# Kernel optimization log

Measured on AMD Instinct MI355X. Metric: run time of the kernel, lower is better.

Reference implementation:

```python
import jax, jax.numpy as jnp
import numpy as np


def setup_inputs() -> dict:
    key = jax.random.key(0)
    k1, k2, k3, k4, k5, k6 = jax.random.split(key, 6)
    N, M = 4096, 4096      # data matrix
    K, D = 2048, 1024      # parameter matrix K x K, similarity matrix K x D
    Npair = 128            # size of i/j index subsets
    return {
        "actual": jax.random.normal(k1, (N, M), dtype=jnp.float32),
        "prediction": jax.random.normal(k2, (N, M), dtype=jnp.float32),
        "lamb": jnp.asarray(0.1, dtype=jnp.float32),
        "P": jax.random.normal(k3, (K, K), dtype=jnp.float32),
        "S": jax.random.normal(k4, (K, D), dtype=jnp.float32),
        "i_indices": jax.random.randint(k5, (Npair,), 0, K, dtype=jnp.int64),
        "j_indices": jax.random.randint(k6, (Npair,), 0, K, dtype=jnp.int64),
    }


def _safe_norm_rows(diff):
    # L2 norm over last axis with a zero-safe sqrt (grad is 0 at exactly-0 diffs,
    # matching torch's subgradient convention for .norm()).
    d2 = jnp.sum(diff * diff, axis=-1)
    pos = d2 > 0
    return jnp.sqrt(jnp.where(pos, d2, 1.0)) * pos


def reference(actual, prediction, lamb, P, S, i_indices, j_indices):
    # (p > 0) * clamp(p, min=0) == relu(p)
    Pp = jnp.maximum(P, 0.0)
    # penalty term: ||relu(P)||_F
    penalty = jnp.linalg.norm(Pp)
    # pairwise parameter-similarity penalty:
    # sum_{i in I, j in J} relu(P)[i,j] * || S[i,:] - S[j,:] ||_2
    Si = S[i_indices]                       # [Ni, D]
    Sj = S[j_indices]                       # [Nj, D]
    diff = Si[:, None, :] - Sj[None, :, :]  # [Ni, Nj, D]
    norms = _safe_norm_rows(diff)           # [Ni, Nj]
    Pij = Pp[i_indices[:, None], j_indices[None, :]]  # [Ni, Nj]
    parameter_penalty = jnp.sum(Pij * norms)
    data_term = jnp.linalg.norm(actual - prediction)
    return data_term + lamb * (penalty + parameter_penalty)
```

## Files before the change

kernel.cpp:

```cpp
#include <hip/hip_runtime.h>
#include <math.h>

#define BR 1024
#define BP 1024
#define TPB 256

__device__ __forceinline__ float waveReduceSum(float v) {
    #pragma unroll
    for (int off = 32; off > 0; off >>= 1)
        v += __shfl_down(v, off, 64);
    return v;
}

__global__ __launch_bounds__(256, 8)
void fused_kernel(const float* __restrict__ a,
                  const float* __restrict__ p,
                  const float* __restrict__ Pm,
                  const float* __restrict__ S,
                  const int* __restrict__ ii,
                  const int* __restrict__ jj,
                  float* __restrict__ ws,
                  long nAP, long nP, int Npair, int D, int K)
{
    __shared__ float sm0[4], sm1[4];
    const int wave = threadIdx.x >> 6;
    const int lane = threadIdx.x & 63;
    const int bid  = blockIdx.x;

    if (bid < BP) {
        const int totalPairs = Npair * Npair;
        const int base = bid * 16 + wave * 4;
        float local = 0.f;

        if (base < totalPairs && D == 1024 && (base % Npair) + 3 < Npair) {
            const int i  = base / Npair;
            const int j0 = base - i * Npair;
            const int ri = ii[i];
            const float4* Si4 = (const float4*)(S + (long)ri * D);
            float4 x0 = Si4[lane];
            float4 x1 = Si4[lane + 64];
            float4 x2 = Si4[lane + 128];
            float4 x3 = Si4[lane + 192];
            const long riK = (long)ri * K;

            float d2q[4];
            int   rjq[4];
            #pragma unroll
            for (int q = 0; q < 4; ++q) {
                const int rj = jj[j0 + q];
                rjq[q] = rj;
                const float4* Sj4 = (const float4*)(S + (long)rj * D);
                float4 y0 = Sj4[lane];
                float4 y1 = Sj4[lane + 64];
                float4 y2 = Sj4[lane + 128];
                float4 y3 = Sj4[lane + 192];
                float d2 = 0.f, e;
                e = x0.x - y0.x; d2 += e * e;
                e = x0.y - y0.y; d2 += e * e;
                e = x0.z - y0.z; d2 += e * e;
                e = x0.w - y0.w; d2 += e * e;
                e = x1.x - y1.x; d2 += e * e;
                e = x1.y - y1.y; d2 += e * e;
                e = x1.z - y1.z; d2 += e * e;
                e = x1.w - y1.w; d2 += e * e;
                e = x2.x - y2.x; d2 += e * e;
                e = x2.y - y2.y; d2 += e * e;
                e = x2.z - y2.z; d2 += e * e;
                e = x2.w - y2.w; d2 += e * e;
                e = x3.x - y3.x; d2 += e * e;
                e = x3.y - y3.y; d2 += e * e;
                e = x3.z - y3.z; d2 += e * e;
                e = x3.w - y3.w; d2 += e * e;
                d2q[q] = d2;
            }
            #pragma unroll
            for (int q = 0; q < 4; ++q)
                d2q[q] = waveReduceSum(d2q[q]);
            if (lane == 0) {
                #pragma unroll
                for (int q = 0; q < 4; ++q)
                    if (d2q[q] > 0.f)
                        local += fmaxf(Pm[riK + rjq[q]], 0.f) * sqrtf(d2q[q]);
            }
        } else {
            #pragma unroll
            for (int q = 0; q < 4; ++q) {
                int pair = base + q;
                if (pair < totalPairs) {
                    int i = pair / Npair;
                    int j = pair - i * Npair;
                    int ri = ii[i];
                    int rj = jj[j];
                    const float* Si = S + (long)ri * D;
                    const float* Sj = S + (long)rj * D;
                    float d2 = 0.f;
                    for (int c = lane; c < D; c += 64) {
                        float e = Si[c] - Sj[c];
                        d2 += e * e;
                    }
                    d2 = waveReduceSum(d2);
                    if (lane == 0 && d2 > 0.f)
                        local += fmaxf(Pm[(long)ri * K + rj], 0.f) * sqrtf(d2);
                }
            }
        }
        if (lane == 0) sm0[wave] = local;
        __syncthreads();
        if (threadIdx.x == 0)
            ws[2 * BR + bid] = sm0[0] + sm0[1] + sm0[2] + sm0[3];
    } else {
        const int rb = bid - BP;
        const long tid    = (long)rb * TPB + threadIdx.x;
        const long stride = (long)BR * TPB;

        const float4* a4 = (const float4*)a;
        const float4* p4 = (const float4*)p;
        long n4 = nAP >> 2;

        float s0a = 0.f, s0b = 0.f, s0c = 0.f, s0d = 0.f;
        long i = tid;
        for (; i + 3 * stride < n4; i += 4 * stride) {
            float4 av0 = a4[i];
            float4 av1 = a4[i + stride];
            float4 av2 = a4[i + 2 * stride];
            float4 av3 = a4[i + 3 * stride];
            float4 pv0 = p4[i];
            float4 pv1 = p4[i + stride];
            float4 pv2 = p4[i + 2 * stride];
            float4 pv3 = p4[i + 3 * stride];
            float d;
            d = av0.x - pv0.x; s0a += d * d;
            d = av0.y - pv0.y; s0a += d * d;
            d = av0.z - pv0.z; s0a += d * d;
            d = av0.w - pv0.w; s0a += d * d;
            d = av1.x - pv1.x; s0b += d * d;
            d = av1.y - pv1.y; s0b += d * d;
            d = av1.z - pv1.z; s0b += d * d;
            d = av1.w - pv1.w; s0b += d * d;
            d = av2.x - pv2.x; s0c += d * d;
            d = av2.y - pv2.y; s0c += d * d;
            d = av2.z - pv2.z; s0c += d * d;
            d = av2.w - pv2.w; s0c += d * d;
            d = av3.x - pv3.x; s0d += d * d;
            d = av3.y - pv3.y; s0d += d * d;
            d = av3.z - pv3.z; s0d += d * d;
            d = av3.w - pv3.w; s0d += d * d;
        }
        for (; i < n4; i += stride) {
            float4 av = a4[i], pv = p4[i];
            float d;
            d = av.x - pv.x; s0a += d * d;
            d = av.y - pv.y; s0a += d * d;
            d = av.z - pv.z; s0a += d * d;
            d = av.w - pv.w; s0a += d * d;
        }

        const float4* P4 = (const float4*)Pm;
        long nP4 = nP >> 2;
        float s1a = 0.f, s1b = 0.f;
        i = tid;
        for (; i + stride < nP4; i += 2 * stride) {
            float4 v0 = P4[i];
            float4 v1 = P4[i + stride];
            float r;
            r = fmaxf(v0.x, 0.f); s1a += r * r;
            r = fmaxf(v0.y, 0.f); s1a += r * r;
            r = fmaxf(v0.z, 0.f); s1a += r * r;
            r = fmaxf(v0.w, 0.f); s1a += r * r;
            r = fmaxf(v1.x, 0.f); s1b += r * r;
            r = fmaxf(v1.y, 0.f); s1b += r * r;
            r = fmaxf(v1.z, 0.f); s1b += r * r;
            r = fmaxf(v1.w, 0.f); s1b += r * r;
        }
        for (; i < nP4; i += stride) {
            float4 v = P4[i];
            float r;
            r = fmaxf(v.x, 0.f); s1a += r * r;
            r = fmaxf(v.y, 0.f); s1a += r * r;
            r = fmaxf(v.z, 0.f); s1a += r * r;
            r = fmaxf(v.w, 0.f); s1a += r * r;
        }

        float s0 = waveReduceSum(s0a + s0b + s0c + s0d);
        float s1 = waveReduceSum(s1a + s1b);
        if (lane == 0) { sm0[wave] = s0; sm1[wave] = s1; }
        __syncthreads();
        if (threadIdx.x == 0) {
            ws[rb]      = sm0[0] + sm0[1] + sm0[2] + sm0[3];
            ws[BR + rb] = sm1[0] + sm1[1] + sm1[2] + sm1[3];
        }
    }
}

__global__ void finalize_kernel(const float* __restrict__ ws,
                                const float* __restrict__ lamb,
                                float* __restrict__ out)
{
    float a0 = 0.f, a1 = 0.f, a2 = 0.f;
    for (int i = threadIdx.x; i < BR; i += TPB) {
        a0 += ws[i];
        a1 += ws[BR + i];
    }
    for (int i = threadIdx.x; i < BP; i += TPB)
        a2 += ws[2 * BR + i];

    a0 = waveReduceSum(a0);
    a1 = waveReduceSum(a1);
    a2 = waveReduceSum(a2);

    __shared__ float m0[4], m1[4], m2[4];
    int wave = threadIdx.x >> 6;
    int lane = threadIdx.x & 63;
    if (lane == 0) { m0[wave] = a0; m1[wave] = a1; m2[wave] = a2; }
    __syncthreads();
    if (threadIdx.x == 0) {
        float A0 = m0[0] + m0[1] + m0[2] + m0[3];
        float A1 = m1[0] + m1[1] + m1[2] + m1[3];
        float A2 = m2[0] + m2[1] + m2[2] + m2[3];
        out[0] = sqrtf(A0) + lamb[0] * (sqrtf(A1) + A2);
    }
}

extern "C" void kernel_launch(void* const* d_in, const int* in_sizes, int n_in,
                              void* d_out, int out_size, void* d_ws, size_t ws_size,
                              hipStream_t stream) {
    const float* actual = (const float*)d_in[0];
    const float* pred   = (const float*)d_in[1];
    const float* lamb   = (const float*)d_in[2];
    const float* Pm     = (const float*)d_in[3];
    const float* S      = (const float*)d_in[4];
    const int*   ii     = (const int*)d_in[5];
    const int*   jj     = (const int*)d_in[6];
    float* out = (float*)d_out;
    float* ws  = (float*)d_ws;

    long nAP   = in_sizes[0];
    long nP    = in_sizes[3];
    int  K     = (int)lround(sqrt((double)nP));
    int  Npair = in_sizes[5];
    int  D     = (int)(in_sizes[4] / K);

    fused_kernel<<<BP + BR, TPB, 0, stream>>>(actual, pred, Pm, S, ii, jj, ws,
                                              nAP, nP, Npair, D, K);
    finalize_kernel<<<1, TPB, 0, stream>>>(ws, lamb, out);
}
```

Measured before the change: 35.73 us.

## Merge pair and streaming work into every block instead of splitting blocks by role

Each of the 2048 blocks now does a grid-strided share of the data-term and relu(P) norm reductions and then computes two S-row-pair distances per wave. Before, 1024 blocks did only the pair work and 1024 did only the streaming reduction. The aim is to balance load so no group of blocks idles or becomes the critical tail, and to spread the bandwidth-bound streaming across all blocks. The finalize kernel now reads the partials with float4 loads. Every block now carries the gather-latency pair work after its streaming loop, which could lengthen per-block time.

New measurement: 37.66 us. 1.05x slower.

```diff
diff --git a/kernel.cpp b/kernel.cpp
--- a/kernel.cpp
+++ b/kernel.cpp
@@ -1,8 +1,7 @@
 #include <hip/hip_runtime.h>
 #include <math.h>
 
-#define BR 1024
-#define BP 1024
+#define NB  2048
 #define TPB 256
 
 __device__ __forceinline__ float waveReduceSum(float v) {
@@ -12,7 +11,7 @@
     return v;
 }
 
-__global__ __launch_bounds__(256, 8)
+__global__ __launch_bounds__(TPB, 8)
 void fused_kernel(const float* __restrict__ a,
                   const float* __restrict__ p,
                   const float* __restrict__ Pm,
@@ -22,173 +21,161 @@
                   float* __restrict__ ws,
                   long nAP, long nP, int Npair, int D, int K)
 {
-    __shared__ float sm0[4], sm1[4];
+    __shared__ float sm0[4], sm1[4], sm2[4];
     const int wave = threadIdx.x >> 6;
     const int lane = threadIdx.x & 63;
     const int bid  = blockIdx.x;
 
-    if (bid < BP) {
-        const int totalPairs = Npair * Npair;
-        const int base = bid * 16 + wave * 4;
-        float local = 0.f;
-
-        if (base < totalPairs && D == 1024 && (base % Npair) + 3 < Npair) {
-            const int i  = base / Npair;
-            const int j0 = base - i * Npair;
-            const int ri = ii[i];
-            const float4* Si4 = (const float4*)(S + (long)ri * D);
-            float4 x0 = Si4[lane];
-            float4 x1 = Si4[lane + 64];
-            float4 x2 = Si4[lane + 128];
-            float4 x3 = Si4[lane + 192];
-            const long riK = (long)ri * K;
-
-            float d2q[4];
-            int   rjq[4];
-            #pragma unroll
-            for (int q = 0; q < 4; ++q) {
-                const int rj = jj[j0 + q];
-                rjq[q] = rj;
-                const float4* Sj4 = (const float4*)(S + (long)rj * D);
-                float4 y0 = Sj4[lane];
-                float4 y1 = Sj4[lane + 64];
-                float4 y2 = Sj4[lane + 128];
-                float4 y3 = Sj4[lane + 192];
-                float d2 = 0.f, e;
-                e = x0.x - y0.x; d2 += e * e;
-                e = x0.y - y0.y; d2 += e * e;
-                e = x0.z - y0.z; d2 += e * e;
-                e = x0.w - y0.w; d2 += e * e;
-                e = x1.x - y1.x; d2 += e * e;
-                e = x1.y - y1.y; d2 += e * e;
-                e = x1.z - y1.z; d2 += e * e;
-                e = x1.w - y1.w; d2 += e * e;
-                e = x2.x - y2.x; d2 += e * e;
-                e = x2.y - y2.y; d2 += e * e;
-                e = x2.z - y2.z; d2 += e * e;
-                e = x2.w - y2.w; d2 += e * e;
-                e = x3.x - y3.x; d2 += e * e;
-                e = x3.y - y3.y; d2 += e * e;
-                e = x3.z - y3.z; d2 += e * e;
-                e = x3.w - y3.w; d2 += e * e;
-                d2q[q] = d2;
+    const long tid    = (long)bid * TPB + threadIdx.x;
+    const long stride = (long)NB * TPB;
+
+    const float4* a4 = (const float4*)a;
+    const float4* p4 = (const float4*)p;
+    const long n4 = nAP >> 2;
+
+    float s0a = 0.f, s0b = 0.f, s0c = 0.f, s0d = 0.f;
+    long i = tid;
+    for (; i + 3 * stride < n4; i += 4 * stride) {
+        float4 av0 = a4[i];
+        float4 av1 = a4[i + stride];
+        float4 av2 = a4[i + 2 * stride];
+        float4 av3 = a4[i + 3 * stride];
+        float4 pv0 = p4[i];
+        float4 pv1 = p4[i + stride];
+        float4 pv2 = p4[i + 2 * stride];
+        float4 pv3 = p4[i + 3 * stride];
+        float d;
+        d = av0.x - pv0.x; s0a += d * d;
+        d = av0.y - pv0.y; s0a += d * d;
+        d = av0.z - pv0.z; s0a += d * d;
+        d = av0.w - pv0.w; s0a += d * d;
+        d = av1.x - pv1.x; s0b += d * d;
+        d = av1.y - pv1.y; s0b += d * d;
+        d = av1.z - pv1.z; s0b += d * d;
+        d = av1.w - pv1.w; s0b += d * d;
+        d = av2.x - pv2.x; s0c += d * d;
+        d = av2.y - pv2.y; s0c += d * d;
+        d = av2.z - pv2.z; s0c += d * d;
+        d = av2.w - pv2.w; s0c += d * d;
+        d = av3.x - pv3.x; s0d += d * d;
+        d = av3.y - pv3.y; s0d += d * d;
+        d = av3.z - pv3.z; s0d += d * d;
+        d = av3.w - pv3.w; s0d += d * d;
+    }
+    for (; i < n4; i += stride) {
+        float4 av = a4[i], pv = p4[i];
+        float d;
+        d = av.x - pv.x; s0a += d * d;
+        d = av.y - pv.y; s0a += d * d;
+        d = av.z - pv.z; s0a += d * d;
+        d = av.w - pv.w; s0a += d * d;
+    }
+
+    const float4* P4 = (const float4*)Pm;
+    const long nP4 = nP >> 2;
+    float s1a = 0.f, s1b = 0.f;
+    i = tid;
+    for (; i + stride < nP4; i += 2 * stride) {
+        float4 v0 = P4[i];
+        float4 v1 = P4[i + stride];
+        float r;
+        r = fmaxf(v0.x, 0.f); s1a += r * r;
+        r = fmaxf(v0.y, 0.f); s1a += r * r;
+        r = fmaxf(v0.z, 0.f); s1a += r * r;
+        r = fmaxf(v0.w, 0.f); s1a += r * r;
+        r = fmaxf(v1.x, 0.f); s1b += r * r;
+        r = fmaxf(v1.y, 0.f); s1b += r * r;
+        r = fmaxf(v1.z, 0.f); s1b += r * r;
+        r = fmaxf(v1.w, 0.f); s1b += r * r;
+    }
+    for (; i < nP4; i += stride) {
+        float4 v = P4[i];
+        float r;
+        r = fmaxf(v.x, 0.f); s1a += r * r;
+        r = fmaxf(v.y, 0.f); s1a += r * r;
+        r = fmaxf(v.z, 0.f); s1a += r * r;
+        r = fmaxf(v.w, 0.f); s1a += r * r;
+    }
+
+    float s0 = waveReduceSum(s0a + s0b + s0c + s0d);
+    float s1 = waveReduceSum(s1a + s1b);
+    if (lane == 0) { sm0[wave] = s0; sm1[wave] = s1; }
+
+    const long totalPairs = (long)Npair * Npair;
+    const long base = ((long)bid * 4 + wave) * 2;
+    float local = 0.f;
+
+    if (base < totalPairs && D == 1024 && (Npair % 2) == 0) {
+        const int ig = (int)(base / Npair);
+        const int j0 = (int)(base - (long)ig * Npair);
+        const int ri = ii[ig];
+        const float4* Si4 = (const float4*)(S + (long)ri * D);
+        float4 x0 = Si4[lane];
+        float4 x1 = Si4[lane + 64];
+        float4 x2 = Si4[lane + 128];
+        float4 x3 = Si4[lane + 192];
+        const long riK = (long)ri * K;
+
+        float d2q[2];
+        int   rjq[2];
+        #pragma unroll
+        for (int q = 0; q < 2; ++q) {
+            const int rj = jj[j0 + q];
+            rjq[q] = rj;
+            const float4* Sj4 = (const float4*)(S + (long)rj * D);
+            float4 y0 = Sj4[lane];
+            float4 y1 = Sj4[lane + 64];
+            float4 y2 = Sj4[lane + 128];
+            float4 y3 = Sj4[lane + 192];
+            float d2 = 0.f, e;
+            e = x0.x - y0.x; d2 += e * e;
+            e = x0.y - y0.y; d2 += e * e;
+            e = x0.z - y0.z; d2 += e * e;
+            e = x0.w - y0.w; d2 += e * e;
+            e = x1.x - y1.x; d2 += e * e;
+            e = x1.y - y1.y; d2 += e * e;
+            e = x1.z - y1.z; d2 += e * e;
+            e = x1.w - y1.w; d2 += e * e;
+            e = x2.x - y2.x; d2 += e * e;
+            e = x2.y - y2.y; d2 += e * e;
+            e = x2.z - y2.z; d2 += e * e;
+            e = x2.w - y2.w; d2 += e * e;
+            e = x3.x - y3.x; d2 += e * e;
+            e = x3.y - y3.y; d2 += e * e;
+            e = x3.z - y3.z; d2 += e * e;
+            e = x3.w - y3.w; d2 += e * e;
+            d2q[q] = d2;
+        }
+        d2q[0] = waveReduceSum(d2q[0]);
+        d2q[1] = waveReduceSum(d2q[1]);
+        if (lane == 0) {
+            if (d2q[0] > 0.f) local += fmaxf(Pm[riK + rjq[0]], 0.f) * sqrtf(d2q[0]);
+            if (d2q[1] > 0.f) local += fmaxf(Pm[riK + rjq[1]], 0.f) * sqrtf(d2q[1]);
+        }
+    } else {
+        for (long pr = base; pr < base + 2 && pr < totalPairs; ++pr) {
+            int ig = (int)(pr / Npair);
+            int j  = (int)(pr - (long)ig * Npair);
+            int ri = ii[ig];
+            int rj = jj[j];
+            const float* Si = S + (long)ri * D;
+            const float* Sj = S + (long)rj * D;
+            float d2 = 0.f;
+            for (int c = lane; c < D; c += 64) {
+                float e = Si[c] - Sj[c];
+                d2 += e * e;
             }
-            #pragma unroll
-            for (int q = 0; q < 4; ++q)
-                d2q[q] = waveReduceSum(d2q[q]);
-            if (lane == 0) {
-                #pragma unroll
-                for (int q = 0; q < 4; ++q)
-                    if (d2q[q] > 0.f)
-                        local += fmaxf(Pm[riK + rjq[q]], 0.f) * sqrtf(d2q[q]);
-            }
-        } else {
-            #pragma unroll
-            for (int q = 0; q < 4; ++q) {
-                int pair = base + q;
-                if (pair < totalPairs) {
-                    int i = pair / Npair;
-                    int j = pair - i * Npair;
-                    int ri = ii[i];
-                    int rj = jj[j];
-                    const float* Si = S + (long)ri * D;
-                    const float* Sj = S + (long)rj * D;
-                    float d2 = 0.f;
-                    for (int c = lane; c < D; c += 64) {
-                        float e = Si[c] - Sj[c];
-                        d2 += e * e;
-                    }
-                    d2 = waveReduceSum(d2);
-                    if (lane == 0 && d2 > 0.f)
-                        local += fmaxf(Pm[(long)ri * K + rj], 0.f) * sqrtf(d2);
-                }
-            }
+            d2 = waveReduceSum(d2);
+            if (lane == 0 && d2 > 0.f)
+                local += fmaxf(Pm[(long)ri * K + rj], 0.f) * sqrtf(d2);
         }
-        if (lane == 0) sm0[wave] = local;
-        __syncthreads();
-        if (threadIdx.x == 0)
-            ws[2 * BR + bid] = sm0[0] + sm0[1] + sm0[2] + sm0[3];
-    } else {
-        const int rb = bid - BP;
-        const long tid    = (long)rb * TPB + threadIdx.x;
-        const long stride = (long)BR * TPB;
-
-        const float4* a4 = (const float4*)a;
-        const float4* p4 = (const float4*)p;
-        long n4 = nAP >> 2;
-
-        float s0a = 0.f, s0b = 0.f, s0c = 0.f, s0d = 0.f;
-        long i = tid;
-        for (; i + 3 * stride < n4; i += 4 * stride) {
-            float4 av0 = a4[i];
-            float4 av1 = a4[i + stride];
-            float4 av2 = a4[i + 2 * stride];
-            float4 av3 = a4[i + 3 * stride];
-            float4 pv0 = p4[i];
-            float4 pv1 = p4[i + stride];
-            float4 pv2 = p4[i + 2 * stride];
-            float4 pv3 = p4[i + 3 * stride];
-            float d;
-            d = av0.x - pv0.x; s0a += d * d;
-            d = av0.y - pv0.y; s0a += d * d;
-            d = av0.z - pv0.z; s0a += d * d;
-            d = av0.w - pv0.w; s0a += d * d;
-            d = av1.x - pv1.x; s0b += d * d;
-            d = av1.y - pv1.y; s0b += d * d;
-            d = av1.z - pv1.z; s0b += d * d;
-            d = av1.w - pv1.w; s0b += d * d;
-            d = av2.x - pv2.x; s0c += d * d;
-            d = av2.y - pv2.y; s0c += d * d;
-            d = av2.z - pv2.z; s0c += d * d;
-            d = av2.w - pv2.w; s0c += d * d;
-            d = av3.x - pv3.x; s0d += d * d;
-            d = av3.y - pv3.y; s0d += d * d;
-            d = av3.z - pv3.z; s0d += d * d;
-            d = av3.w - pv3.w; s0d += d * d;
-        }
-        for (; i < n4; i += stride) {
-            float4 av = a4[i], pv = p4[i];
-            float d;
-            d = av.x - pv.x; s0a += d * d;
-            d = av.y - pv.y; s0a += d * d;
-            d = av.z - pv.z; s0a += d * d;
-            d = av.w - pv.w; s0a += d * d;
-        }
-
-        const float4* P4 = (const float4*)Pm;
-        long nP4 = nP >> 2;
-        float s1a = 0.f, s1b = 0.f;
-        i = tid;
-        for (; i + stride < nP4; i += 2 * stride) {
-            float4 v0 = P4[i];
-            float4 v1 = P4[i + stride];
-            float r;
-            r = fmaxf(v0.x, 0.f); s1a += r * r;
-            r = fmaxf(v0.y, 0.f); s1a += r * r;
-            r = fmaxf(v0.z, 0.f); s1a += r * r;
-            r = fmaxf(v0.w, 0.f); s1a += r * r;
-            r = fmaxf(v1.x, 0.f); s1b += r * r;
-            r = fmaxf(v1.y, 0.f); s1b += r * r;
-            r = fmaxf(v1.z, 0.f); s1b += r * r;
-            r = fmaxf(v1.w, 0.f); s1b += r * r;
-        }
-        for (; i < nP4; i += stride) {
-            float4 v = P4[i];
-            float r;
-            r = fmaxf(v.x, 0.f); s1a += r * r;
-            r = fmaxf(v.y, 0.f); s1a += r * r;
-            r = fmaxf(v.z, 0.f); s1a += r * r;
-            r = fmaxf(v.w, 0.f); s1a += r * r;
-        }
-
-        float s0 = waveReduceSum(s0a + s0b + s0c + s0d);
-        float s1 = waveReduceSum(s1a + s1b);
-        if (lane == 0) { sm0[wave] = s0; sm1[wave] = s1; }
-        __syncthreads();
-        if (threadIdx.x == 0) {
-            ws[rb]      = sm0[0] + sm0[1] + sm0[2] + sm0[3];
-            ws[BR + rb] = sm1[0] + sm1[1] + sm1[2] + sm1[3];
-        }
+    }
+    if (lane == 0) sm2[wave] = local;
+    __syncthreads();
+    if (threadIdx.x == 0) {
+        ws[bid]          = sm0[0] + sm0[1] + sm0[2] + sm0[3];
+        ws[NB + bid]     = sm1[0] + sm1[1] + sm1[2] + sm1[3];
+        ws[2 * NB + bid] = sm2[0] + sm2[1] + sm2[2] + sm2[3];
     }
 }
 
@@ -197,12 +184,15 @@
                                 float* __restrict__ out)
 {
     float a0 = 0.f, a1 = 0.f, a2 = 0.f;
-    for (int i = threadIdx.x; i < BR; i += TPB) {
-        a0 += ws[i];
-        a1 += ws[BR + i];
-    }
-    for (int i = threadIdx.x; i < BP; i += TPB)
-        a2 += ws[2 * BR + i];
+    const float4* w4 = (const float4*)ws;
+    for (int i = threadIdx.x; i < NB / 4; i += TPB) {
+        float4 v = w4[i];
+        a0 += v.x + v.y + v.z + v.w;
+        float4 u = w4[NB / 4 + i];
+        a1 += u.x + u.y + u.z + u.w;
+        float4 t = w4[2 * (NB / 4) + i];
+        a2 += t.x + t.y + t.z + t.w;
+    }
 
     a0 = waveReduceSum(a0);
     a1 = waveReduceSum(a1);
@@ -240,7 +230,7 @@
     int  Npair = in_sizes[5];
     int  D     = (int)(in_sizes[4] / K);
 
-    fused_kernel<<<BP + BR, TPB, 0, stream>>>(actual, pred, Pm, S, ii, jj, ws,
-                                              nAP, nP, Npair, D, K);
+    fused_kernel<<<NB, TPB, 0, stream>>>(actual, pred, Pm, S, ii, jj, ws,
+                                         nAP, nP, Npair, D, K);
     finalize_kernel<<<1, TPB, 0, stream>>>(ws, lamb, out);
 }
```
